# Performance work log

Measured on AMD Instinct MI355X. Metric: run time of the kernel, lower is better.

The kernel has to match this reference:

```python
import jax, jax.numpy as jnp
import numpy as np

BLOCK_Q = 64
BLOCK_KV = 64
TOPK_RATIO = 0.125


def setup_inputs() -> dict:
    key = jax.random.key(0)
    k1, k2, k3 = jax.random.split(key, 3)
    B, H, L, D = 1, 16, 8192, 64
    q = jax.random.normal(k1, (B, H, L, D), dtype=jnp.float32)
    k = jax.random.normal(k2, (B, H, L, D), dtype=jnp.float32)
    v = jax.random.normal(k3, (B, H, L, D), dtype=jnp.float32)
    return {"q": q, "k": k, "v": v}


def _sparse_lut(q, k):
    # get_sparse_map: block mean-pool q and mean-centered k, score blocks, top-k key blocks
    B, H, L, D = q.shape
    Mb, Nb = L // BLOCK_Q, L // BLOCK_KV
    q_pool = q.reshape(B, H, Mb, BLOCK_Q, D).mean(axis=3)          # [B,H,Mb,D]
    smooth_k = k - k.mean(axis=-2, keepdims=True)
    k_pool = smooth_k.reshape(B, H, Nb, BLOCK_KV, D).mean(axis=3)  # [B,H,Nb,D]
    pred = jnp.einsum('bhmd,bhnd->bhmn', q_pool, k_pool)           # [B,H,Mb,Nb]
    topk = int(TOPK_RATIO * Nb)
    _, lut = jax.lax.top_k(pred, topk)                             # [B,H,Mb,topk]
    return lut


def reference(q, k, v):
    B, H, L, D = q.shape
    Mb, Nb = L // BLOCK_Q, L // BLOCK_KV
    lut = _sparse_lut(q, k)                                        # [B,H,Mb,T] int32
    T = lut.shape[-1]
    sm_scale = D ** -0.5

    kb = k.reshape(B, H, Nb, BLOCK_KV, D)
    vb = v.reshape(B, H, Nb, BLOCK_KV, D)
    bi = jnp.arange(B)[:, None, None, None]
    hi = jnp.arange(H)[None, :, None, None]
    # gather selected KV blocks per query block: [B,H,Mb,T,BLOCK_KV,D]
    k_sel = kb[bi, hi, lut].reshape(B, H, Mb, T * BLOCK_KV, D)
    v_sel = vb[bi, hi, lut].reshape(B, H, Mb, T * BLOCK_KV, D)

    qb = q.reshape(B, H, Mb, BLOCK_Q, D)
    s = jnp.einsum('bhmqd,bhmkd->bhmqk', qb, k_sel) * sm_scale     # [B,H,Mb,BQ,T*BKV]
    p = jax.nn.softmax(s, axis=-1)
    o = jnp.einsum('bhmqk,bhmkd->bhmqd', p, v_sel)
    return o.reshape(B, H, L, D)
```

## Files before the change

### kernel.cpp

```cpp
#include <hip/hip_runtime.h>
#include <hip/hip_bf16.h>


#define H_  16
#define L_  8192
#define D_  64
#define MB_ 128
#define NB_ 128
#define TK_ 16
#define ST_ 72
#define PST 72

typedef __bf16 bf16x8 __attribute__((ext_vector_type(8)));
typedef float  f32x4  __attribute__((ext_vector_type(4)));
typedef unsigned short u16x8 __attribute__((ext_vector_type(8)));

union BFU { __hip_bfloat16 h; unsigned short u; };

static __device__ inline unsigned short f2bfu(float f) {
  BFU c; c.h = __float2bfloat16(f); return c.u;
}

__device__ unsigned short g_qb[(size_t)H_ * L_ * D_];
__device__ unsigned short g_kb[(size_t)H_ * L_ * D_];
__device__ unsigned short g_vt[(size_t)H_ * D_ * L_];
__device__ float g_qpool[H_ * NB_ * 64];
__device__ float g_kpool[H_ * NB_ * 64];
__device__ int   g_lut[H_ * MB_ * TK_];

static __device__ inline void cvt8_2(const float4& f0, const float4& f1,
                                     unsigned short* dst) {
  u16x8 s;
  s[0] = f2bfu(f0.x); s[1] = f2bfu(f0.y); s[2] = f2bfu(f0.z); s[3] = f2bfu(f0.w);
  s[4] = f2bfu(f1.x); s[5] = f2bfu(f1.y); s[6] = f2bfu(f1.z); s[7] = f2bfu(f1.w);
  *(u16x8*)dst = s;
}

static __device__ inline void cvt8_2s(const float4& f0, const float4& f1,
                                      unsigned short* dst, float sc) {
  u16x8 s;
  s[0] = f2bfu(f0.x * sc); s[1] = f2bfu(f0.y * sc);
  s[2] = f2bfu(f0.z * sc); s[3] = f2bfu(f0.w * sc);
  s[4] = f2bfu(f1.x * sc); s[5] = f2bfu(f1.y * sc);
  s[6] = f2bfu(f1.z * sc); s[7] = f2bfu(f1.w * sc);
  *(u16x8*)dst = s;
}

__global__ __launch_bounds__(256)
void fusedpool_kernel(const float* __restrict__ q,
                      const float* __restrict__ k,
                      const float* __restrict__ v) {
  __shared__ float qt[64 * 64];
  __shared__ float kt[64 * 64];
  __shared__ __align__(16) unsigned short vt_s[64 * ST_];
  __shared__ float pq[4][64], pk[4][64];

  const int b = blockIdx.x;
  const int h = b >> 7, n = b & 127;
  const int t = threadIdx.x;
  const int r = t >> 2, c = (t & 3) * 16;
  const size_t base = (size_t)b * 4096 + r * 64 + c;
  const float cs = 0.18033688011112042f;

  float4 qf0 = *(const float4*)(q + base),      qf1 = *(const float4*)(q + base + 4);
  float4 qf2 = *(const float4*)(q + base + 8),  qf3 = *(const float4*)(q + base + 12);
  float4 kf0 = *(const float4*)(k + base),      kf1 = *(const float4*)(k + base + 4);
  float4 kf2 = *(const float4*)(k + base + 8),  kf3 = *(const float4*)(k + base + 12);
  float4 vf0 = *(const float4*)(v + base),      vf1 = *(const float4*)(v + base + 4);
  float4 vf2 = *(const float4*)(v + base + 8),  vf3 = *(const float4*)(v + base + 12);

  cvt8_2s(qf0, qf1, g_qb + base, cs);  cvt8_2s(qf2, qf3, g_qb + base + 8, cs);
  cvt8_2(kf0, kf1, g_kb + base);       cvt8_2(kf2, kf3, g_kb + base + 8);
  cvt8_2(vf0, vf1, vt_s + r * ST_ + c);
  cvt8_2(vf2, vf3, vt_s + r * ST_ + c + 8);

  *(float4*)(qt + r * 64 + c)      = qf0; *(float4*)(qt + r * 64 + c + 4)  = qf1;
  *(float4*)(qt + r * 64 + c + 8)  = qf2; *(float4*)(qt + r * 64 + c + 12) = qf3;
  *(float4*)(kt + r * 64 + c)      = kf0; *(float4*)(kt + r * 64 + c + 4)  = kf1;
  *(float4*)(kt + r * 64 + c + 8)  = kf2; *(float4*)(kt + r * 64 + c + 12) = kf3;
  __syncthreads();

  const int col = t & 63, g = t >> 6;
  float sq = 0.f, sk = 0.f;
  for (int rr = g * 16; rr < g * 16 + 16; ++rr) {
    sq += qt[rr * 64 + col];
    sk += kt[rr * 64 + col];
  }
  pq[g][col] = sq; pk[g][col] = sk;

  u16x8 va, vb;
  #pragma unroll
  for (int i = 0; i < 8; ++i) va[i] = vt_s[(c + i) * ST_ + r];
  #pragma unroll
  for (int i = 0; i < 8; ++i) vb[i] = vt_s[(c + 8 + i) * ST_ + r];
  const size_t vo = ((size_t)h * 64 + r) * (size_t)L_ + (size_t)n * 64 + c;
  *(u16x8*)(g_vt + vo)     = va;
  *(u16x8*)(g_vt + vo + 8) = vb;

  __syncthreads();
  if (t < 64) {
    g_qpool[b * 64 + t] = (pq[0][t] + pq[1][t] + pq[2][t] + pq[3][t]) * (1.f / 64.f);
    g_kpool[b * 64 + t] = (pk[0][t] + pk[1][t] + pk[2][t] + pk[3][t]) * (1.f / 64.f);
  }
}

__global__ void center_kernel() {
  __shared__ float part[4][64];
  const int h = blockIdx.x;
  const int d = threadIdx.x & 63;
  const int s = threadIdx.x >> 6;
  const int base = h * NB_ * 64 + d;
  float sum = 0.f;
  for (int n = s * 32; n < s * 32 + 32; ++n) sum += g_kpool[base + n * 64];
  part[s][d] = sum;
  __syncthreads();
  const float mean = (part[0][d] + part[1][d] + part[2][d] + part[3][d]) * (1.f / NB_);
  for (int n = s * 32; n < s * 32 + 32; ++n) g_kpool[base + n * 64] -= mean;
}

__global__ void topk_kernel() {
  const int b = blockIdx.x;
  const int h = b >> 7;
  const int lane = threadIdx.x;
  const float4* qrow = (const float4*)(g_qpool + b * 64);
  const float4* k0 = (const float4*)(g_kpool + (h * NB_ + lane) * 64);
  const float4* k1 = (const float4*)(g_kpool + (h * NB_ + lane + 64) * 64);
  float v0 = 0.f, v1 = 0.f;
  for (int i = 0; i < 16; ++i) {
    float4 qv = qrow[i];
    float4 a = k0[i];
    float4 c = k1[i];
    v0 += qv.x * a.x + qv.y * a.y + qv.z * a.z + qv.w * a.w;
    v1 += qv.x * c.x + qv.y * c.y + qv.z * c.z + qv.w * c.w;
  }
  for (int t = 0; t < TK_; ++t) {
    float bv; int bi;
    if (v0 >= v1) { bv = v0; bi = lane; } else { bv = v1; bi = lane + 64; }
    for (int mask = 1; mask < 64; mask <<= 1) {
      float ov = __shfl_xor(bv, mask, 64);
      int   oi = __shfl_xor(bi, mask, 64);
      if (ov > bv || (ov == bv && oi < bi)) { bv = ov; bi = oi; }
    }
    if (lane == 0) g_lut[b * TK_ + t] = bi;
    if (bi == lane) v0 = -3.0e38f;
    else if (bi == lane + 64) v1 = -3.0e38f;
  }
}

__global__ __launch_bounds__(256, 4)
void attn_kernel(float* __restrict__ out) {
  __shared__ __align__(16) unsigned short Qs[64 * ST_];
  __shared__ __align__(16) unsigned short Ks[64 * ST_];
  __shared__ __align__(16) unsigned short Vt[64 * ST_];
  __shared__ __align__(16) unsigned short Pw[4][16 * PST];

  const int blk = blockIdx.x;
  const int h = blk & 15, m = blk >> 4;
  const int t = threadIdx.x;
  const int w = t >> 6;
  const int lane = t & 63;
  const int l16 = lane & 15, quad = lane >> 4;
  const int srow = t >> 3, scol = (t & 7) * 8;
  const int vd = t >> 2, vc = (t & 3) * 16;

  const unsigned short* qg = g_qb + ((size_t)h * L_ + (size_t)m * 64) * D_;
  *(u16x8*)(Qs + srow * ST_ + scol)        = *(const u16x8*)(qg + t * 8);
  *(u16x8*)(Qs + (32 + srow) * ST_ + scol) = *(const u16x8*)(qg + 2048 + t * 8);
  __syncthreads();

  const bf16x8 aq0 = *(const bf16x8*)&Qs[(16 * w + l16) * ST_ + quad * 8];
  const bf16x8 aq1 = *(const bf16x8*)&Qs[(16 * w + l16) * ST_ + 32 + quad * 8];

  f32x4 o[4];
  #pragma unroll
  for (int n4 = 0; n4 < 4; ++n4) o[n4] = (f32x4){0.f, 0.f, 0.f, 0.f};
  float mrow[4] = {-1e30f, -1e30f, -1e30f, -1e30f};
  float lsum[4] = {0.f, 0.f, 0.f, 0.f};

  const int* my_lut = g_lut + (h * MB_ + m) * TK_;
  const unsigned short* vg = g_vt + (size_t)h * D_ * L_;

  const int kb0 = my_lut[0] & 127;
  const size_t koff0 = ((size_t)h * L_ + (size_t)kb0 * 64) * D_;
  u16x8 kx0 = *(const u16x8*)(g_kb + koff0 + t * 8);
  u16x8 kx1 = *(const u16x8*)(g_kb + koff0 + 2048 + t * 8);
  u16x8 vx0 = *(const u16x8*)(vg + (size_t)vd * L_ + kb0 * 64 + vc);
  u16x8 vx1 = *(const u16x8*)(vg + (size_t)vd * L_ + kb0 * 64 + vc + 8);

  for (int j = 0; j < TK_; ++j) {
    *(u16x8*)(Ks + srow * ST_ + scol)        = kx0;
    *(u16x8*)(Ks + (32 + srow) * ST_ + scol) = kx1;
    *(u16x8*)(Vt + vd * ST_ + vc)     = vx0;
    *(u16x8*)(Vt + vd * ST_ + vc + 8) = vx1;
    __syncthreads();

    if (j + 1 < TK_) {
      const int kb = my_lut[j + 1] & 127;
      const size_t koff = ((size_t)h * L_ + (size_t)kb * 64) * D_;
      kx0 = *(const u16x8*)(g_kb + koff + t * 8);
      kx1 = *(const u16x8*)(g_kb + koff + 2048 + t * 8);
      vx0 = *(const u16x8*)(vg + (size_t)vd * L_ + kb * 64 + vc);
      vx1 = *(const u16x8*)(vg + (size_t)vd * L_ + kb * 64 + vc + 8);
    }

    f32x4 acc[4];
    #pragma unroll
    for (int n4 = 0; n4 < 4; ++n4) {
      bf16x8 b0 = *(const bf16x8*)&Ks[(n4 * 16 + l16) * ST_ + quad * 8];
      bf16x8 b1 = *(const bf16x8*)&Ks[(n4 * 16 + l16) * ST_ + 32 + quad * 8];
      f32x4 z = (f32x4){0.f, 0.f, 0.f, 0.f};
      z = __builtin_amdgcn_mfma_f32_16x16x32_bf16(aq0, b0, z, 0, 0, 0);
      z = __builtin_amdgcn_mfma_f32_16x16x32_bf16(aq1, b1, z, 0, 0, 0);
      acc[n4] = z;
    }

    float p[4][4];
    #pragma unroll
    for (int r = 0; r < 4; ++r) {
      float x0r = acc[0][r], x1r = acc[1][r];
      float x2r = acc[2][r], x3r = acc[3][r];
      float mx = fmaxf(fmaxf(x0r, x1r), fmaxf(x2r, x3r));
      #pragma unroll
      for (int mask = 1; mask < 16; mask <<= 1)
        mx = fmaxf(mx, __shfl_xor(mx, mask, 64));
      const float nm = fmaxf(mrow[r], mx);
      const float alpha = exp2f(mrow[r] - nm);
      mrow[r] = nm;
      p[0][r] = exp2f(x0r - nm); p[1][r] = exp2f(x1r - nm);
      p[2][r] = exp2f(x2r - nm); p[3][r] = exp2f(x3r - nm);
      lsum[r] = lsum[r] * alpha + (p[0][r] + p[1][r] + p[2][r] + p[3][r]);
      #pragma unroll
      for (int n4 = 0; n4 < 4; ++n4) o[n4][r] *= alpha;
    }

    unsigned short* pw = &Pw[w][0];
    #pragma unroll
    for (int n4 = 0; n4 < 4; ++n4)
      #pragma unroll
      for (int r = 0; r < 4; ++r)
        pw[(quad * 4 + r) * PST + n4 * 16 + l16] = f2bfu(p[n4][r]);

    asm volatile("s_waitcnt lgkmcnt(0)" ::: "memory");
    __builtin_amdgcn_sched_barrier(0);

    const bf16x8 pa0 = *(const bf16x8*)&pw[l16 * PST + quad * 8];
    const bf16x8 pa1 = *(const bf16x8*)&pw[l16 * PST + 32 + quad * 8];

    #pragma unroll
    for (int n4 = 0; n4 < 4; ++n4) {
      bf16x8 v0f = *(const bf16x8*)&Vt[(n4 * 16 + l16) * ST_ + quad * 8];
      bf16x8 v1f = *(const bf16x8*)&Vt[(n4 * 16 + l16) * ST_ + 32 + quad * 8];
      o[n4] = __builtin_amdgcn_mfma_f32_16x16x32_bf16(pa0, v0f, o[n4], 0, 0, 0);
      o[n4] = __builtin_amdgcn_mfma_f32_16x16x32_bf16(pa1, v1f, o[n4], 0, 0, 0);
    }
    __syncthreads();
  }

  #pragma unroll
  for (int r = 0; r < 4; ++r) {
    float rs = lsum[r];
    #pragma unroll
    for (int mask = 1; mask < 16; mask <<= 1)
      rs += __shfl_xor(rs, mask, 64);
    lsum[r] = rs;
  }
  const size_t obase = ((size_t)h * L_ + (size_t)m * 64) * D_;
  #pragma unroll
  for (int n4 = 0; n4 < 4; ++n4) {
    #pragma unroll
    for (int r = 0; r < 4; ++r) {
      const int qrow = 16 * w + quad * 4 + r;
      out[obase + (size_t)qrow * 64 + n4 * 16 + l16] = o[n4][r] / lsum[r];
    }
  }
}

extern "C" void kernel_launch(void* const* d_in, const int* in_sizes, int n_in,
                              void* d_out, int out_size, void* d_ws, size_t ws_size,
                              hipStream_t stream) {
  const float* q = (const float*)d_in[0];
  const float* k = (const float*)d_in[1];
  const float* v = (const float*)d_in[2];
  float* out = (float*)d_out;

  fusedpool_kernel<<<H_ * NB_, 256, 0, stream>>>(q, k, v);
  center_kernel<<<H_, 256, 0, stream>>>();
  topk_kernel<<<H_ * MB_, 64, 0, stream>>>();
  attn_kernel<<<H_ * MB_, 256, 0, stream>>>(out);
}
```

Baseline: 270.9 us.

## Load K/V MFMA fragments directly from global into registers, dropping LDS staging

```diff
diff --git a/kernel.cpp b/kernel.cpp
--- a/kernel.cpp
+++ b/kernel.cpp
@@ -149,9 +149,6 @@
 
 __global__ __launch_bounds__(256, 4)
 void attn_kernel(float* __restrict__ out) {
-  __shared__ __align__(16) unsigned short Qs[64 * ST_];
-  __shared__ __align__(16) unsigned short Ks[64 * ST_];
-  __shared__ __align__(16) unsigned short Vt[64 * ST_];
   __shared__ __align__(16) unsigned short Pw[4][16 * PST];
 
   const int blk = blockIdx.x;
@@ -160,16 +157,19 @@
   const int w = t >> 6;
   const int lane = t & 63;
   const int l16 = lane & 15, quad = lane >> 4;
-  const int srow = t >> 3, scol = (t & 7) * 8;
-  const int vd = t >> 2, vc = (t & 3) * 16;
 
   const unsigned short* qg = g_qb + ((size_t)h * L_ + (size_t)m * 64) * D_;
-  *(u16x8*)(Qs + srow * ST_ + scol)        = *(const u16x8*)(qg + t * 8);
-  *(u16x8*)(Qs + (32 + srow) * ST_ + scol) = *(const u16x8*)(qg + 2048 + t * 8);
-  __syncthreads();
-
-  const bf16x8 aq0 = *(const bf16x8*)&Qs[(16 * w + l16) * ST_ + quad * 8];
-  const bf16x8 aq1 = *(const bf16x8*)&Qs[(16 * w + l16) * ST_ + 32 + quad * 8];
+  const unsigned short* qrow = qg + (16 * w + l16) * 64 + quad * 8;
+  const bf16x8 aq0 = *(const bf16x8*)(qrow);
+  const bf16x8 aq1 = *(const bf16x8*)(qrow + 32);
+
+  const unsigned short* kh = g_kb + (size_t)h * L_ * D_;
+  const unsigned short* vh = g_vt + (size_t)h * D_ * L_;
+  const int koffl = l16 * 64 + quad * 8;
+  const int voff0 = (0 * 16 + l16) * L_ + quad * 8;
+  const int voff1 = (1 * 16 + l16) * L_ + quad * 8;
+  const int voff2 = (2 * 16 + l16) * L_ + quad * 8;
+  const int voff3 = (3 * 16 + l16) * L_ + quad * 8;
 
   f32x4 o[4];
   #pragma unroll
@@ -178,40 +178,44 @@
   float lsum[4] = {0.f, 0.f, 0.f, 0.f};
 
   const int* my_lut = g_lut + (h * MB_ + m) * TK_;
-  const unsigned short* vg = g_vt + (size_t)h * D_ * L_;
-
-  const int kb0 = my_lut[0] & 127;
-  const size_t koff0 = ((size_t)h * L_ + (size_t)kb0 * 64) * D_;
-  u16x8 kx0 = *(const u16x8*)(g_kb + koff0 + t * 8);
-  u16x8 kx1 = *(const u16x8*)(g_kb + koff0 + 2048 + t * 8);
-  u16x8 vx0 = *(const u16x8*)(vg + (size_t)vd * L_ + kb0 * 64 + vc);
-  u16x8 vx1 = *(const u16x8*)(vg + (size_t)vd * L_ + kb0 * 64 + vc + 8);
+
+  bf16x8 kf0[4], kf1[4], vf0[4], vf1[4];
+
+  int kb = __builtin_amdgcn_readfirstlane(my_lut[0] & 127);
+  {
+    const unsigned short* kbp = kh + (size_t)kb * 4096;
+    #pragma unroll
+    for (int n4 = 0; n4 < 4; ++n4) {
+      kf0[n4] = *(const bf16x8*)(kbp + n4 * 1024 + koffl);
+      kf1[n4] = *(const bf16x8*)(kbp + n4 * 1024 + koffl + 32);
+    }
+    const unsigned short* vbp = vh + kb * 64;
+    vf0[0] = *(const bf16x8*)(vbp + voff0); vf1[0] = *(const bf16x8*)(vbp + voff0 + 32);
+    vf0[1] = *(const bf16x8*)(vbp + voff1); vf1[1] = *(const bf16x8*)(vbp + voff1 + 32);
+    vf0[2] = *(const bf16x8*)(vbp + voff2); vf1[2] = *(const bf16x8*)(vbp + voff2 + 32);
+    vf0[3] = *(const bf16x8*)(vbp + voff3); vf1[3] = *(const bf16x8*)(vbp + voff3 + 32);
+  }
 
   for (int j = 0; j < TK_; ++j) {
-    *(u16x8*)(Ks + srow * ST_ + scol)        = kx0;
-    *(u16x8*)(Ks + (32 + srow) * ST_ + scol) = kx1;
-    *(u16x8*)(Vt + vd * ST_ + vc)     = vx0;
-    *(u16x8*)(Vt + vd * ST_ + vc + 8) = vx1;
-    __syncthreads();
+    const int kbn = (j + 1 < TK_)
+        ? __builtin_amdgcn_readfirstlane(my_lut[j + 1] & 127) : kb;
+
+    f32x4 acc[4];
+    #pragma unroll
+    for (int n4 = 0; n4 < 4; ++n4) {
+      f32x4 z = (f32x4){0.f, 0.f, 0.f, 0.f};
+      z = __builtin_amdgcn_mfma_f32_16x16x32_bf16(aq0, kf0[n4], z, 0, 0, 0);
+      z = __builtin_amdgcn_mfma_f32_16x16x32_bf16(aq1, kf1[n4], z, 0, 0, 0);
+      acc[n4] = z;
+    }
 
     if (j + 1 < TK_) {
-      const int kb = my_lut[j + 1] & 127;
-      const size_t koff = ((size_t)h * L_ + (size_t)kb * 64) * D_;
-      kx0 = *(const u16x8*)(g_kb + koff + t * 8);
-      kx1 = *(const u16x8*)(g_kb + koff + 2048 + t * 8);
-      vx0 = *(const u16x8*)(vg + (size_t)vd * L_ + kb * 64 + vc);
-      vx1 = *(const u16x8*)(vg + (size_t)vd * L_ + kb * 64 + vc + 8);
-    }
-
-    f32x4 acc[4];
-    #pragma unroll
-    for (int n4 = 0; n4 < 4; ++n4) {
-      bf16x8 b0 = *(const bf16x8*)&Ks[(n4 * 16 + l16) * ST_ + quad * 8];
-      bf16x8 b1 = *(const bf16x8*)&Ks[(n4 * 16 + l16) * ST_ + 32 + quad * 8];
-      f32x4 z = (f32x4){0.f, 0.f, 0.f, 0.f};
-      z = __builtin_amdgcn_mfma_f32_16x16x32_bf16(aq0, b0, z, 0, 0, 0);
-      z = __builtin_amdgcn_mfma_f32_16x16x32_bf16(aq1, b1, z, 0, 0, 0);
-      acc[n4] = z;
+      const unsigned short* kbp = kh + (size_t)kbn * 4096;
+      #pragma unroll
+      for (int n4 = 0; n4 < 4; ++n4) {
+        kf0[n4] = *(const bf16x8*)(kbp + n4 * 1024 + koffl);
+        kf1[n4] = *(const bf16x8*)(kbp + n4 * 1024 + koffl + 32);
+      }
     }
 
     float p[4][4];
@@ -248,12 +252,18 @@
 
     #pragma unroll
     for (int n4 = 0; n4 < 4; ++n4) {
-      bf16x8 v0f = *(const bf16x8*)&Vt[(n4 * 16 + l16) * ST_ + quad * 8];
-      bf16x8 v1f = *(const bf16x8*)&Vt[(n4 * 16 + l16) * ST_ + 32 + quad * 8];
-      o[n4] = __builtin_amdgcn_mfma_f32_16x16x32_bf16(pa0, v0f, o[n4], 0, 0, 0);
-      o[n4] = __builtin_amdgcn_mfma_f32_16x16x32_bf16(pa1, v1f, o[n4], 0, 0, 0);
-    }
-    __syncthreads();
+      o[n4] = __builtin_amdgcn_mfma_f32_16x16x32_bf16(pa0, vf0[n4], o[n4], 0, 0, 0);
+      o[n4] = __builtin_amdgcn_mfma_f32_16x16x32_bf16(pa1, vf1[n4], o[n4], 0, 0, 0);
+    }
+
+    if (j + 1 < TK_) {
+      const unsigned short* vbp = vh + kbn * 64;
+      vf0[0] = *(const bf16x8*)(vbp + voff0); vf1[0] = *(const bf16x8*)(vbp + voff0 + 32);
+      vf0[1] = *(const bf16x8*)(vbp + voff1); vf1[1] = *(const bf16x8*)(vbp + voff1 + 32);
+      vf0[2] = *(const bf16x8*)(vbp + voff2); vf1[2] = *(const bf16x8*)(vbp + voff2 + 32);
+      vf0[3] = *(const bf16x8*)(vbp + voff3); vf1[3] = *(const bf16x8*)(vbp + voff3 + 32);
+    }
+    kb = kbn;
   }
 
   #pragma unroll
@@ -269,8 +279,8 @@
   for (int n4 = 0; n4 < 4; ++n4) {
     #pragma unroll
     for (int r = 0; r < 4; ++r) {
-      const int qrow = 16 * w + quad * 4 + r;
-      out[obase + (size_t)qrow * 64 + n4 * 16 + l16] = o[n4][r] / lsum[r];
+      const int qrow_o = 16 * w + quad * 4 + r;
+      out[obase + (size_t)qrow_o * 64 + n4 * 16 + l16] = o[n4][r] / lsum[r];
     }
   }
 }
```

Measured after the change: 424.2 us. 56.6% more time.
